# Optimization experiments

Hardware: AMD Instinct MI355X
Metric: run time of the kernel (lower is better)

Reference implementation:

```python
import jax, jax.numpy as jnp
import numpy as np

N, E, G = 50000, 800000, 64
IN_CH, HID = 64, 64


def setup_inputs() -> dict:
    key = jax.random.key(0)
    ks = jax.random.split(key, 16)
    inp = {
        "x": jax.random.normal(ks[0], (N, IN_CH), dtype=jnp.float32),
        "edge_index": jax.random.randint(ks[1], (2, E), 0, N, dtype=jnp.int64),
        "edge_weight": jax.random.uniform(ks[2], (E,), dtype=jnp.float32),
        "batch": jnp.sort(jax.random.randint(ks[3], (N,), 0, G, dtype=jnp.int64)),
        "W1": jax.random.normal(ks[4], (IN_CH, HID), dtype=jnp.float32) / np.sqrt(IN_CH),
        "b1": jnp.zeros((HID,), dtype=jnp.float32),
        "W2": jax.random.normal(ks[5], (HID, HID), dtype=jnp.float32) / np.sqrt(HID),
        "b2": jnp.zeros((HID,), dtype=jnp.float32),
        "W3": jax.random.normal(ks[6], (HID, HID), dtype=jnp.float32) / np.sqrt(HID),
        "b3": jnp.zeros((HID,), dtype=jnp.float32),
        "lw1": jax.random.normal(ks[7], (HID, HID // 2), dtype=jnp.float32) / np.sqrt(HID),
        "lb1": jnp.zeros((HID // 2,), dtype=jnp.float32),
        "lw2": jax.random.normal(ks[8], (HID // 2, HID // 4), dtype=jnp.float32) / np.sqrt(HID // 2),
        "lb2": jnp.zeros((HID // 4,), dtype=jnp.float32),
        "lw3": jax.random.normal(ks[9], (HID // 4, 1), dtype=jnp.float32) / np.sqrt(HID // 4),
        "lb3": jnp.zeros((1,), dtype=jnp.float32),
    }
    return inp


def _gcn_layer(x, W, b, src, dst, ew):
    # GCNConv with normalize=False: transform, gather at src, weight, scatter-add at dst, + bias
    h = x @ W                                  # [N, HID]
    msg = h[src] * ew[:, None]                 # [E, HID] gather + edge weighting
    agg = jax.ops.segment_sum(msg, dst, num_segments=N)  # [N, HID] scatter-add
    return agg + b


def reference(x, edge_index, edge_weight, batch,
              W1, b1, W2, b2, W3, b3,
              lw1, lb1, lw2, lb2, lw3, lb3):
    src, dst = edge_index[0], edge_index[1]
    h = jax.nn.relu(_gcn_layer(x, W1, b1, src, dst, edge_weight))
    h = jax.nn.relu(_gcn_layer(h, W2, b2, src, dst, edge_weight))
    h = jax.nn.relu(_gcn_layer(h, W3, b3, src, dst, edge_weight))
    # global mean pool over graphs
    sums = jax.ops.segment_sum(h, batch, num_segments=G)          # [G, HID]
    cnts = jax.ops.segment_sum(jnp.ones((N,), h.dtype), batch, num_segments=G)
    pooled = sums / jnp.clip(cnts, 1.0)[:, None]
    # MLP head (dropout is identity in eval mode)
    z = jax.nn.relu(pooled @ lw1 + lb1)
    z = jax.nn.relu(z @ lw2 + lb2)
    return z @ lw3 + lb3                       # [G, 1]
```

## Files before the change

### kernel.cpp

```cpp
#include <hip/hip_runtime.h>
#include <hip/hip_bf16.h>
#include <hip/hip_fp16.h>


#define HID 64
#define KNBLK 256

__global__ __launch_bounds__(256) void histA_kernel(const int* __restrict__ ei,
                                                    int* __restrict__ counts,
                                                    int E, int K, int chunk) {
    __shared__ int hist[256];
    int t = threadIdx.x, b = blockIdx.x;
    hist[t] = 0;
    __syncthreads();
    int s = b * chunk, e1 = min(E, s + chunk);
    for (int i = s + t; i < e1; i += 256)
        atomicAdd(&hist[ei[E + i] >> 8], 1);
    __syncthreads();
    if (t < K) counts[b * K + t] = hist[t];
}

__global__ __launch_bounds__(256) void scanB1_kernel(int* __restrict__ counts,
                                                     int* __restrict__ btot, int K) {
    __shared__ int sh[256];
    int k = blockIdx.x, t = threadIdx.x;
    int v = counts[t * K + k];
    sh[t] = v;
    __syncthreads();
    #pragma unroll
    for (int d = 1; d < 256; d <<= 1) {
        int add = (t >= d) ? sh[t - d] : 0;
        __syncthreads();
        sh[t] += add;
        __syncthreads();
    }
    counts[t * K + k] = sh[t] - v;
    if (t == 255) btot[k] = sh[255];
}

__global__ __launch_bounds__(256) void scanB2_kernel(const int* __restrict__ btot,
                                                     int* __restrict__ bb0, int K) {
    __shared__ int sh[256];
    int t = threadIdx.x;
    int v = (t < K) ? btot[t] : 0;
    sh[t] = v;
    __syncthreads();
    #pragma unroll
    for (int d = 1; d < 256; d <<= 1) {
        int add = (t >= d) ? sh[t - d] : 0;
        __syncthreads();
        sh[t] += add;
        __syncthreads();
    }
    if (t < K) bb0[t] = sh[t] - v;
    if (t == 255) bb0[K] = sh[255];
}

__global__ __launch_bounds__(256) void passB_kernel(const int* __restrict__ ei,
                                                    const float* __restrict__ ew,
                                                    const int* __restrict__ counts,
                                                    const int* __restrict__ bb0,
                                                    int4* __restrict__ ebuf,
                                                    int E, int K, int chunk) {
    __shared__ int lcur[256];
    int t = threadIdx.x, b = blockIdx.x;
    lcur[t] = 0;
    __syncthreads();
    int s = b * chunk, e1 = min(E, s + chunk);
    for (int i = s + t; i < e1; i += 256) {
        int src = ei[i];
        int dst = ei[E + i];
        float w = ew[i];
        int k = dst >> 8;
        int idx = atomicAdd(&lcur[k], 1);
        int slot = bb0[k] + counts[b * K + k] + idx;
        ebuf[slot] = make_int4(src, __float_as_int(w), dst, 0);
    }
}

__global__ __launch_bounds__(256) void passC_kernel(const int4* __restrict__ ebuf,
                                                    const int* __restrict__ bb0,
                                                    int2* __restrict__ csr,
                                                    int* __restrict__ offs,
                                                    int N, int E, int K) {
    __shared__ int ldeg[256];
    __shared__ int sh[256];
    __shared__ int lofs[256];
    int b = blockIdx.x, t = threadIdx.x;
    int gb0 = bb0[b], gb1 = bb0[b + 1];
    int cnt = gb1 - gb0;
    int base = b << 8;
    ldeg[t] = 0;
    __syncthreads();
    for (int i = t; i < cnt; i += 256)
        atomicAdd(&ldeg[ebuf[gb0 + i].z & 255], 1);
    __syncthreads();
    int v = ldeg[t];
    sh[t] = v;
    __syncthreads();
    #pragma unroll
    for (int d = 1; d < 256; d <<= 1) {
        int add = (t >= d) ? sh[t - d] : 0;
        __syncthreads();
        sh[t] += add;
        __syncthreads();
    }
    lofs[t] = sh[t] - v;
    int nInB = min(256, N - base);
    if (t < nInB) offs[base + t] = gb0 + lofs[t];
    if (b == K - 1 && t == 0) offs[N] = E;
    __syncthreads();
    for (int i = t; i < cnt; i += 256) {
        int4 r = ebuf[gb0 + i];
        int d = r.z & 255;
        int pos = atomicAdd(&lofs[d], 1);
        csr[gb0 + pos] = make_int2(r.x, r.y);
    }
}

__global__ __launch_bounds__(256) void conv_kernel(const float* __restrict__ in,
                                                   __half* __restrict__ out, int n4) {
    int i = blockIdx.x * 256 + threadIdx.x;
    if (i < n4) {
        const float4 v = *reinterpret_cast<const float4*>(in + (size_t)i * 4);
        __half2 a = __float22half2_rn(make_float2(v.x, v.y));
        __half2 b = __float22half2_rn(make_float2(v.z, v.w));
        uint2 u;
        u.x = __builtin_bit_cast(unsigned int, a);
        u.y = __builtin_bit_cast(unsigned int, b);
        *reinterpret_cast<uint2*>(out + (size_t)i * 4) = u;
    }
}

__global__ __launch_bounds__(256) void agg_fused_kernel(const __half* __restrict__ prev,
                                                        const int2* __restrict__ csr,
                                                        const int* __restrict__ offs,
                                                        const float* __restrict__ W,
                                                        const float* __restrict__ bias,
                                                        __half* __restrict__ out, int N) {
    __shared__ float Wl[64 * 64];
    __shared__ float bl[64];
    for (int i = threadIdx.x; i < 64 * 64; i += 256) Wl[i] = W[i];
    if (threadIdx.x < 64) bl[threadIdx.x] = bias[threadIdx.x];
    __syncthreads();

    int g = (blockIdx.x * 256 + threadIdx.x) >> 4;
    int l = threadIdx.x & 15;
    if (g >= N) return;

    int e0 = offs[g], e1 = offs[g + 1];
    float4 acc = make_float4(0.f, 0.f, 0.f, 0.f);

    #define GLOAD(R, F0, F1)                                                         \
        const uint2 u##F0 = *reinterpret_cast<const uint2*>(                         \
            prev + (size_t)(R).x * 64 + l * 4);                                      \
        const float2 F0 = __half22float2(__builtin_bit_cast(__half2, u##F0.x));      \
        const float2 F1 = __half22float2(__builtin_bit_cast(__half2, u##F0.y));

    int e = e0;
    for (; e + 4 <= e1; e += 4) {
        int2 r0 = csr[e + 0];
        int2 r1 = csr[e + 1];
        int2 r2 = csr[e + 2];
        int2 r3 = csr[e + 3];
        GLOAD(r0, fa0, fa1);
        GLOAD(r1, fb0, fb1);
        GLOAD(r2, fc0, fc1);
        GLOAD(r3, fd0, fd1);
        const float w0 = __int_as_float(r0.y);
        const float w1 = __int_as_float(r1.y);
        const float w2 = __int_as_float(r2.y);
        const float w3 = __int_as_float(r3.y);
        acc.x = fmaf(w0, fa0.x, acc.x); acc.y = fmaf(w0, fa0.y, acc.y);
        acc.z = fmaf(w0, fa1.x, acc.z); acc.w = fmaf(w0, fa1.y, acc.w);
        acc.x = fmaf(w1, fb0.x, acc.x); acc.y = fmaf(w1, fb0.y, acc.y);
        acc.z = fmaf(w1, fb1.x, acc.z); acc.w = fmaf(w1, fb1.y, acc.w);
        acc.x = fmaf(w2, fc0.x, acc.x); acc.y = fmaf(w2, fc0.y, acc.y);
        acc.z = fmaf(w2, fc1.x, acc.z); acc.w = fmaf(w2, fc1.y, acc.w);
        acc.x = fmaf(w3, fd0.x, acc.x); acc.y = fmaf(w3, fd0.y, acc.y);
        acc.z = fmaf(w3, fd1.x, acc.z); acc.w = fmaf(w3, fd1.y, acc.w);
    }
    for (; e < e1; ++e) {
        int2 r = csr[e];
        GLOAD(r, fe0, fe1);
        const float w = __int_as_float(r.y);
        acc.x = fmaf(w, fe0.x, acc.x);
        acc.y = fmaf(w, fe0.y, acc.y);
        acc.z = fmaf(w, fe1.x, acc.z);
        acc.w = fmaf(w, fe1.y, acc.w);
    }
    #undef GLOAD

    const float b0 = bl[l * 4 + 0], b1_ = bl[l * 4 + 1];
    const float b2_ = bl[l * 4 + 2], b3_ = bl[l * 4 + 3];
    float4 o = make_float4(b0, b1_, b2_, b3_);
    #pragma unroll
    for (int k2 = 0; k2 < 16; ++k2) {
        float c0 = __shfl(acc.x, k2, 16);
        float c1 = __shfl(acc.y, k2, 16);
        float c2 = __shfl(acc.z, k2, 16);
        float c3 = __shfl(acc.w, k2, 16);
        const float4 w0 = *reinterpret_cast<const float4*>(Wl + (4 * k2 + 0) * 64 + l * 4);
        const float4 w1 = *reinterpret_cast<const float4*>(Wl + (4 * k2 + 1) * 64 + l * 4);
        const float4 w2 = *reinterpret_cast<const float4*>(Wl + (4 * k2 + 2) * 64 + l * 4);
        const float4 w3 = *reinterpret_cast<const float4*>(Wl + (4 * k2 + 3) * 64 + l * 4);
        o.x = fmaf(c0, w0.x, o.x); o.y = fmaf(c0, w0.y, o.y);
        o.z = fmaf(c0, w0.z, o.z); o.w = fmaf(c0, w0.w, o.w);
        o.x = fmaf(c1, w1.x, o.x); o.y = fmaf(c1, w1.y, o.y);
        o.z = fmaf(c1, w1.z, o.z); o.w = fmaf(c1, w1.w, o.w);
        o.x = fmaf(c2, w2.x, o.x); o.y = fmaf(c2, w2.y, o.y);
        o.z = fmaf(c2, w2.z, o.z); o.w = fmaf(c2, w2.w, o.w);
        o.x = fmaf(c3, w3.x, o.x); o.y = fmaf(c3, w3.y, o.y);
        o.z = fmaf(c3, w3.z, o.z); o.w = fmaf(c3, w3.w, o.w);
    }
    __half2 oa = __float22half2_rn(make_float2(fmaxf(o.x, 0.f), fmaxf(o.y, 0.f)));
    __half2 ob = __float22half2_rn(make_float2(fmaxf(o.z, 0.f), fmaxf(o.w, 0.f)));
    uint2 u;
    u.x = __builtin_bit_cast(unsigned int, oa);
    u.y = __builtin_bit_cast(unsigned int, ob);
    *reinterpret_cast<uint2*>(out + (size_t)g * 64 + l * 4) = u;
}

__global__ __launch_bounds__(256) void pool_kernel(const __half* __restrict__ a,
                                                   const int* __restrict__ batch,
                                                   float* __restrict__ sums,
                                                   float* __restrict__ cnts, int N) {
    int c = threadIdx.x & 63;
    int sub = threadIdx.x >> 6;
    int chunk = (N + gridDim.x - 1) / gridDim.x;
    int start = blockIdx.x * chunk;
    int end = min(N, start + chunk);
    int curg = -1;
    float acc = 0.f, cacc = 0.f;
    for (int n = start + sub; n < end; n += 4) {
        int g = batch[n];
        if (g != curg) {
            if (curg >= 0) {
                atomicAdd(&sums[curg * 64 + c], acc);
                if (c == 0) atomicAdd(&cnts[curg], cacc);
            }
            curg = g; acc = 0.f; cacc = 0.f;
        }
        acc += __half2float(a[(size_t)n * 64 + c]);
        cacc += 1.f;
    }
    if (curg >= 0) {
        atomicAdd(&sums[curg * 64 + c], acc);
        if (c == 0) atomicAdd(&cnts[curg], cacc);
    }
}

__global__ __launch_bounds__(256) void head_kernel(const float* __restrict__ sums,
                                                   const float* __restrict__ cnts,
                                                   const float* __restrict__ lw1,
                                                   const float* __restrict__ lb1,
                                                   const float* __restrict__ lw2,
                                                   const float* __restrict__ lb2,
                                                   const float* __restrict__ lw3,
                                                   const float* __restrict__ lb3,
                                                   float* __restrict__ out, int G) {
    __shared__ float pooled[64 * 64];
    __shared__ float z1[64 * 32];
    __shared__ float z2[64 * 16];
    int tid = threadIdx.x;
    for (int i = tid; i < G * 64; i += 256) {
        int g = i >> 6;
        float cn = cnts[g];
        cn = (cn < 1.f) ? 1.f : cn;
        pooled[i] = sums[i] / cn;
    }
    __syncthreads();
    for (int i = tid; i < G * 32; i += 256) {
        int g = i >> 5, j = i & 31;
        float acc = lb1[j];
        #pragma unroll
        for (int k = 0; k < 64; ++k) acc = fmaf(pooled[g * 64 + k], lw1[k * 32 + j], acc);
        z1[i] = fmaxf(acc, 0.f);
    }
    __syncthreads();
    for (int i = tid; i < G * 16; i += 256) {
        int g = i >> 4, j = i & 15;
        float acc = lb2[j];
        #pragma unroll
        for (int k = 0; k < 32; ++k) acc = fmaf(z1[g * 32 + k], lw2[k * 16 + j], acc);
        z2[i] = fmaxf(acc, 0.f);
    }
    __syncthreads();
    if (tid < G) {
        float acc = lb3[0];
        #pragma unroll
        for (int k = 0; k < 16; ++k) acc = fmaf(z2[tid * 16 + k], lw3[k], acc);
        out[tid] = acc;
    }
}

static inline size_t align256(size_t x) { return (x + 255) & ~(size_t)255; }

extern "C" void kernel_launch(void* const* d_in, const int* in_sizes, int n_in,
                              void* d_out, int out_size, void* d_ws, size_t ws_size,
                              hipStream_t stream) {
    const float* x     = (const float*)d_in[0];
    const int*   ei    = (const int*)d_in[1];
    const float* ew    = (const float*)d_in[2];
    const int*   batch = (const int*)d_in[3];
    const float* W1 = (const float*)d_in[4];
    const float* b1 = (const float*)d_in[5];
    const float* W2 = (const float*)d_in[6];
    const float* b2 = (const float*)d_in[7];
    const float* W3 = (const float*)d_in[8];
    const float* b3 = (const float*)d_in[9];
    const float* lw1 = (const float*)d_in[10];
    const float* lb1 = (const float*)d_in[11];
    const float* lw2 = (const float*)d_in[12];
    const float* lb2 = (const float*)d_in[13];
    const float* lw3 = (const float*)d_in[14];
    const float* lb3 = (const float*)d_in[15];
    float* out = (float*)d_out;

    const int N = in_sizes[0] / 64;
    const int E = in_sizes[2];
    const int G = out_size;
    const int K = (N + 255) >> 8;
    const int chunk = (E + KNBLK - 1) / KNBLK;

    char* w = (char*)d_ws;
    size_t off = 0;
    auto carve = [&](size_t bytes) -> void* {
        void* p = w + off;
        off = align256(off + bytes);
        return p;
    };
    __half* xh    = (__half*)carve((size_t)N * 64 * 2);
    __half* hA    = (__half*)carve((size_t)N * 64 * 2);
    __half* hB    = (__half*)carve((size_t)N * 64 * 2);
    int2*  csr    = (int2*)carve((size_t)E * 8);
    int*   counts = (int*)carve((size_t)KNBLK * K * 4);
    int*   btot   = (int*)carve((size_t)K * 4);
    int*   bb0    = (int*)carve((size_t)(K + 1) * 4);
    int*   offs   = (int*)carve((size_t)(N + 1) * 4);
    float* sums   = (float*)carve((size_t)G * 64 * 4);
    float* cnts   = (float*)carve((size_t)G * 4);
    int4*  ebuf   = (int4*)xh;
    (void)ws_size; (void)n_in;

    hipMemsetAsync(sums, 0, (size_t)G * 64 * 4, stream);
    hipMemsetAsync(cnts, 0, (size_t)G * 4, stream);

    histA_kernel <<<KNBLK, 256, 0, stream>>>(ei, counts, E, K, chunk);
    scanB1_kernel<<<K,     256, 0, stream>>>(counts, btot, K);
    scanB2_kernel<<<1,     256, 0, stream>>>(btot, bb0, K);
    passB_kernel <<<KNBLK, 256, 0, stream>>>(ei, ew, counts, bb0, ebuf, E, K, chunk);
    passC_kernel <<<K,     256, 0, stream>>>(ebuf, bb0, csr, offs, N, E, K);

    const int n4 = N * 64 / 4;
    conv_kernel<<<(n4 + 255) / 256, 256, 0, stream>>>(x, xh, n4);

    const int AGG_BLOCKS = (int)(((size_t)N * 16 + 255) / 256);

    agg_fused_kernel<<<AGG_BLOCKS, 256, 0, stream>>>(xh, csr, offs, W1, b1, hA, N);
    agg_fused_kernel<<<AGG_BLOCKS, 256, 0, stream>>>(hA, csr, offs, W2, b2, hB, N);
    agg_fused_kernel<<<AGG_BLOCKS, 256, 0, stream>>>(hB, csr, offs, W3, b3, hA, N);

    pool_kernel<<<1024, 256, 0, stream>>>(hA, batch, sums, cnts, N);
    head_kernel<<<1, 256, 0, stream>>>(sums, cnts, lw1, lb1, lw2, lb2, lw3, lb3, out, G);
}
```

Measured before the change: 186.6 us.

## Use 8 lanes per node with 16-byte gathers and pack edge sort buffer

The aggregation kernel now assigns 8 lanes per node instead of 16, so each lane gathers 8 half values with one 16-byte load, and the fused 64x64 transform is reorganised around 8-wide shuffles and outputs. Separately, the intermediate edge buffer shrinks from int4 to int2 by packing the low 8 bits of dst into the upper bits of src. This halves the sort buffer traffic and means fewer, wider gather loads, which should improve memory efficiency. The cost is more registers per thread and fewer threads per node. The packing also assumes src fits in 16 bits, but N is 50000, so src can exceed 65535 only if N grows; here it fits.

```diff
diff --git a/kernel.cpp b/kernel.cpp
--- a/kernel.cpp
+++ b/kernel.cpp
@@ -60,7 +60,7 @@
                                                     const float* __restrict__ ew,
                                                     const int* __restrict__ counts,
                                                     const int* __restrict__ bb0,
-                                                    int4* __restrict__ ebuf,
+                                                    int2* __restrict__ ebuf,
                                                     int E, int K, int chunk) {
     __shared__ int lcur[256];
     int t = threadIdx.x, b = blockIdx.x;
@@ -74,11 +74,11 @@
         int k = dst >> 8;
         int idx = atomicAdd(&lcur[k], 1);
         int slot = bb0[k] + counts[b * K + k] + idx;
-        ebuf[slot] = make_int4(src, __float_as_int(w), dst, 0);
-    }
-}
-
-__global__ __launch_bounds__(256) void passC_kernel(const int4* __restrict__ ebuf,
+        ebuf[slot] = make_int2(src | ((dst & 255) << 16), __float_as_int(w));
+    }
+}
+
+__global__ __launch_bounds__(256) void passC_kernel(const int2* __restrict__ ebuf,
                                                     const int* __restrict__ bb0,
                                                     int2* __restrict__ csr,
                                                     int* __restrict__ offs,
@@ -93,7 +93,7 @@
     ldeg[t] = 0;
     __syncthreads();
     for (int i = t; i < cnt; i += 256)
-        atomicAdd(&ldeg[ebuf[gb0 + i].z & 255], 1);
+        atomicAdd(&ldeg[(ebuf[gb0 + i].x >> 16) & 255], 1);
     __syncthreads();
     int v = ldeg[t];
     sh[t] = v;
@@ -111,10 +111,10 @@
     if (b == K - 1 && t == 0) offs[N] = E;
     __syncthreads();
     for (int i = t; i < cnt; i += 256) {
-        int4 r = ebuf[gb0 + i];
-        int d = r.z & 255;
+        int2 r = ebuf[gb0 + i];
+        int d = (r.x >> 16) & 255;
         int pos = atomicAdd(&lofs[d], 1);
-        csr[gb0 + pos] = make_int2(r.x, r.y);
+        csr[gb0 + pos] = make_int2(r.x & 0xFFFF, r.y);
     }
 }
 
@@ -144,18 +144,26 @@
     if (threadIdx.x < 64) bl[threadIdx.x] = bias[threadIdx.x];
     __syncthreads();
 
-    int g = (blockIdx.x * 256 + threadIdx.x) >> 4;
-    int l = threadIdx.x & 15;
+    int g = (blockIdx.x * 256 + threadIdx.x) >> 3;
+    int l = threadIdx.x & 7;
     if (g >= N) return;
 
     int e0 = offs[g], e1 = offs[g + 1];
-    float4 acc = make_float4(0.f, 0.f, 0.f, 0.f);
-
-    #define GLOAD(R, F0, F1)                                                         \
-        const uint2 u##F0 = *reinterpret_cast<const uint2*>(                         \
-            prev + (size_t)(R).x * 64 + l * 4);                                      \
-        const float2 F0 = __half22float2(__builtin_bit_cast(__half2, u##F0.x));      \
-        const float2 F1 = __half22float2(__builtin_bit_cast(__half2, u##F0.y));
+    float acc[8] = {0.f, 0.f, 0.f, 0.f, 0.f, 0.f, 0.f, 0.f};
+
+    #define GLOAD(R, U)                                                              \
+        const uint4 U = *reinterpret_cast<const uint4*>(prev + (size_t)(R).x * 64 + l * 8);
+    #define GACC(U, WW)                                                              \
+        {                                                                            \
+            const float2 f0 = __half22float2(__builtin_bit_cast(__half2, (U).x));    \
+            const float2 f1 = __half22float2(__builtin_bit_cast(__half2, (U).y));    \
+            const float2 f2 = __half22float2(__builtin_bit_cast(__half2, (U).z));    \
+            const float2 f3 = __half22float2(__builtin_bit_cast(__half2, (U).w));    \
+            acc[0] = fmaf((WW), f0.x, acc[0]); acc[1] = fmaf((WW), f0.y, acc[1]);    \
+            acc[2] = fmaf((WW), f1.x, acc[2]); acc[3] = fmaf((WW), f1.y, acc[3]);    \
+            acc[4] = fmaf((WW), f2.x, acc[4]); acc[5] = fmaf((WW), f2.y, acc[5]);    \
+            acc[6] = fmaf((WW), f3.x, acc[6]); acc[7] = fmaf((WW), f3.y, acc[7]);    \
+        }
 
     int e = e0;
     for (; e + 4 <= e1; e += 4) {
@@ -163,62 +171,51 @@
         int2 r1 = csr[e + 1];
         int2 r2 = csr[e + 2];
         int2 r3 = csr[e + 3];
-        GLOAD(r0, fa0, fa1);
-        GLOAD(r1, fb0, fb1);
-        GLOAD(r2, fc0, fc1);
-        GLOAD(r3, fd0, fd1);
-        const float w0 = __int_as_float(r0.y);
-        const float w1 = __int_as_float(r1.y);
-        const float w2 = __int_as_float(r2.y);
-        const float w3 = __int_as_float(r3.y);
-        acc.x = fmaf(w0, fa0.x, acc.x); acc.y = fmaf(w0, fa0.y, acc.y);
-        acc.z = fmaf(w0, fa1.x, acc.z); acc.w = fmaf(w0, fa1.y, acc.w);
-        acc.x = fmaf(w1, fb0.x, acc.x); acc.y = fmaf(w1, fb0.y, acc.y);
-        acc.z = fmaf(w1, fb1.x, acc.z); acc.w = fmaf(w1, fb1.y, acc.w);
-        acc.x = fmaf(w2, fc0.x, acc.x); acc.y = fmaf(w2, fc0.y, acc.y);
-        acc.z = fmaf(w2, fc1.x, acc.z); acc.w = fmaf(w2, fc1.y, acc.w);
-        acc.x = fmaf(w3, fd0.x, acc.x); acc.y = fmaf(w3, fd0.y, acc.y);
-        acc.z = fmaf(w3, fd1.x, acc.z); acc.w = fmaf(w3, fd1.y, acc.w);
+        GLOAD(r0, ua);
+        GLOAD(r1, ub);
+        GLOAD(r2, uc);
+        GLOAD(r3, ud);
+        GACC(ua, __int_as_float(r0.y));
+        GACC(ub, __int_as_float(r1.y));
+        GACC(uc, __int_as_float(r2.y));
+        GACC(ud, __int_as_float(r3.y));
     }
     for (; e < e1; ++e) {
         int2 r = csr[e];
-        GLOAD(r, fe0, fe1);
-        const float w = __int_as_float(r.y);
-        acc.x = fmaf(w, fe0.x, acc.x);
-        acc.y = fmaf(w, fe0.y, acc.y);
-        acc.z = fmaf(w, fe1.x, acc.z);
-        acc.w = fmaf(w, fe1.y, acc.w);
+        GLOAD(r, ue);
+        GACC(ue, __int_as_float(r.y));
     }
     #undef GLOAD
-
-    const float b0 = bl[l * 4 + 0], b1_ = bl[l * 4 + 1];
-    const float b2_ = bl[l * 4 + 2], b3_ = bl[l * 4 + 3];
-    float4 o = make_float4(b0, b1_, b2_, b3_);
-    #pragma unroll
-    for (int k2 = 0; k2 < 16; ++k2) {
-        float c0 = __shfl(acc.x, k2, 16);
-        float c1 = __shfl(acc.y, k2, 16);
-        float c2 = __shfl(acc.z, k2, 16);
-        float c3 = __shfl(acc.w, k2, 16);
-        const float4 w0 = *reinterpret_cast<const float4*>(Wl + (4 * k2 + 0) * 64 + l * 4);
-        const float4 w1 = *reinterpret_cast<const float4*>(Wl + (4 * k2 + 1) * 64 + l * 4);
-        const float4 w2 = *reinterpret_cast<const float4*>(Wl + (4 * k2 + 2) * 64 + l * 4);
-        const float4 w3 = *reinterpret_cast<const float4*>(Wl + (4 * k2 + 3) * 64 + l * 4);
-        o.x = fmaf(c0, w0.x, o.x); o.y = fmaf(c0, w0.y, o.y);
-        o.z = fmaf(c0, w0.z, o.z); o.w = fmaf(c0, w0.w, o.w);
-        o.x = fmaf(c1, w1.x, o.x); o.y = fmaf(c1, w1.y, o.y);
-        o.z = fmaf(c1, w1.z, o.z); o.w = fmaf(c1, w1.w, o.w);
-        o.x = fmaf(c2, w2.x, o.x); o.y = fmaf(c2, w2.y, o.y);
-        o.z = fmaf(c2, w2.z, o.z); o.w = fmaf(c2, w2.w, o.w);
-        o.x = fmaf(c3, w3.x, o.x); o.y = fmaf(c3, w3.y, o.y);
-        o.z = fmaf(c3, w3.z, o.z); o.w = fmaf(c3, w3.w, o.w);
-    }
-    __half2 oa = __float22half2_rn(make_float2(fmaxf(o.x, 0.f), fmaxf(o.y, 0.f)));
-    __half2 ob = __float22half2_rn(make_float2(fmaxf(o.z, 0.f), fmaxf(o.w, 0.f)));
-    uint2 u;
-    u.x = __builtin_bit_cast(unsigned int, oa);
-    u.y = __builtin_bit_cast(unsigned int, ob);
-    *reinterpret_cast<uint2*>(out + (size_t)g * 64 + l * 4) = u;
+    #undef GACC
+
+    float o[8];
+    #pragma unroll
+    for (int j = 0; j < 8; ++j) o[j] = bl[l * 8 + j];
+    #pragma unroll
+    for (int k2 = 0; k2 < 8; ++k2) {
+        float c[8];
+        #pragma unroll
+        for (int j = 0; j < 8; ++j) c[j] = __shfl(acc[j], k2, 8);
+        #pragma unroll
+        for (int j = 0; j < 8; ++j) {
+            const float4 wa = *reinterpret_cast<const float4*>(Wl + (8 * k2 + j) * 64 + l * 8);
+            const float4 wb = *reinterpret_cast<const float4*>(Wl + (8 * k2 + j) * 64 + l * 8 + 4);
+            o[0] = fmaf(c[j], wa.x, o[0]); o[1] = fmaf(c[j], wa.y, o[1]);
+            o[2] = fmaf(c[j], wa.z, o[2]); o[3] = fmaf(c[j], wa.w, o[3]);
+            o[4] = fmaf(c[j], wb.x, o[4]); o[5] = fmaf(c[j], wb.y, o[5]);
+            o[6] = fmaf(c[j], wb.z, o[6]); o[7] = fmaf(c[j], wb.w, o[7]);
+        }
+    }
+    uint4 u;
+    u.x = __builtin_bit_cast(unsigned int,
+          __float22half2_rn(make_float2(fmaxf(o[0], 0.f), fmaxf(o[1], 0.f))));
+    u.y = __builtin_bit_cast(unsigned int,
+          __float22half2_rn(make_float2(fmaxf(o[2], 0.f), fmaxf(o[3], 0.f))));
+    u.z = __builtin_bit_cast(unsigned int,
+          __float22half2_rn(make_float2(fmaxf(o[4], 0.f), fmaxf(o[5], 0.f))));
+    u.w = __builtin_bit_cast(unsigned int,
+          __float22half2_rn(make_float2(fmaxf(o[6], 0.f), fmaxf(o[7], 0.f))));
+    *reinterpret_cast<uint4*>(out + (size_t)g * 64 + l * 8) = u;
 }
 
 __global__ __launch_bounds__(256) void pool_kernel(const __half* __restrict__ a,
@@ -340,7 +337,7 @@
     int*   offs   = (int*)carve((size_t)(N + 1) * 4);
     float* sums   = (float*)carve((size_t)G * 64 * 4);
     float* cnts   = (float*)carve((size_t)G * 4);
-    int4*  ebuf   = (int4*)xh;
+    int2*  ebuf   = (int2*)xh;
     (void)ws_size; (void)n_in;
 
     hipMemsetAsync(sums, 0, (size_t)G * 64 * 4, stream);
@@ -355,7 +352,7 @@
     const int n4 = N * 64 / 4;
     conv_kernel<<<(n4 + 255) / 256, 256, 0, stream>>>(x, xh, n4);
 
-    const int AGG_BLOCKS = (int)(((size_t)N * 16 + 255) / 256);
+    const int AGG_BLOCKS = (int)(((size_t)N * 8 + 255) / 256);
 
     agg_fused_kernel<<<AGG_BLOCKS, 256, 0, stream>>>(xh, csr, offs, W1, b1, hA, N);
     agg_fused_kernel<<<AGG_BLOCKS, 256, 0, stream>>>(hA, csr, offs, W2, b2, hB, N);
```

Measured after the change: 165.9 us. -11.1%, faster.
